# Optimization experiments

Hardware: AMD Instinct MI355X
Metric: run time of the kernel (lower is better)

The kernel has to match this reference:

```python
import jax, jax.numpy as jnp
import numpy as np

D = 1024          # feature dim (x_dim)
C = 32            # n classes (way)
SHOTS = 32
N_SUP = C * SHOTS
Q = 1024
REG = 0.5         # reg_param


def setup_inputs() -> dict:
    key = jax.random.key(0)
    ks = jax.random.split(key, 5)
    support_x = jax.random.normal(ks[0], (N_SUP, D), dtype=jnp.float32)
    query_x = jax.random.normal(ks[1], (Q, D), dtype=jnp.float32)
    labels_idx = (jnp.arange(N_SUP, dtype=jnp.int32) % C)  # every class present, equal shots
    m = jax.random.normal(ks[2], (1, D), dtype=jnp.float32) * 0.01
    kappa = jnp.float32(0.1)
    nu = jnp.float32(D)
    triu_diag = jnp.ones((D,), dtype=jnp.float32)
    triu_lower = jnp.eye(D, dtype=jnp.float32) + 0.01 * jax.random.normal(ks[3], (D, D), dtype=jnp.float32)
    return {"support_x": support_x, "query_x": query_x, "labels_idx": labels_idx,
            "m": m, "kappa": kappa, "nu": nu,
            "triu_diag": triu_diag, "triu_lower": triu_lower}


def _metaqda_fb(support_x, query_x, labels_idx, m, kappa, nu, triu_diag, triu_lower):
    onehot = jax.nn.one_hot(labels_idx, C, dtype=support_x.dtype)      # [N, C]
    Nj = jnp.sum(onehot, axis=0)                                       # [C]
    kappa_ = jnp.abs(kappa) + 1e-6
    nu_ = jnp.maximum(nu, jnp.float32(D - 1 + 1e-6))

    # Cholesky-factor prior scatter matrix: L @ L^T
    lower_mask = jnp.tril(jnp.ones((D, D), dtype=support_x.dtype), k=-1)
    L = jnp.diag(jnp.abs(triu_diag)) + triu_lower * lower_mask
    prior_S = L @ L.T                                                  # [D, D]

    # per-class sums (replaces python loop of rank-1 outer products with GEMMs)
    sum_x = onehot.T @ support_x                                       # [C, D]
    mean_x = sum_x / Nj[:, None]
    # sum_n x x^T per class: contract through [N,C,D] intermediate
    SXX = jnp.einsum('nc,nd,ne->cde', onehot, support_x, support_x)    # [C, D, D]

    kN = kappa_ + Nj                                                   # [C]
    mu = (kappa_ / kN)[:, None] * m + (Nj / kN)[:, None] * mean_x      # [C, D]

    mm = m.T @ m                                                       # [D, D]  (self_outer of [1,D])
    mumu = jnp.einsum('cd,ce->cde', mu, mu)                            # [C, D, D]
    S = prior_S[None] + SXX + kappa_ * mm[None] - kN[:, None, None] * mumu

    scale = (kN + 1.0) / ((nu_ + Nj - D + 1.0) * kN)                   # [C]
    sigma = S * scale[:, None, None]                                   # [C, D, D]

    sigma_inv = (1.0 - REG) * jnp.linalg.inv(sigma) + REG * jnp.eye(D, dtype=sigma.dtype)

    common = nu_ + Nj + 1.0 - D                                        # [C]
    _, logdet = jnp.linalg.slogdet(sigma)
    bias = (jax.lax.lgamma(0.5 * (common + D)) - jax.lax.lgamma(0.5 * common)
            - 0.5 * D * jnp.log(common) - 0.5 * logdet)                # [C]

    diff = query_x[:, None, :] - mu[None, :, :]                        # [Q, C, D]
    dist = jnp.einsum('qcd,cde,qce->qc', diff, sigma_inv, diff)        # [Q, C]
    preds = bias[None, :] - 0.5 * (common + D)[None, :] * jnp.log1p(dist / common[None, :])
    return preds


def reference(support_x, query_x, labels_idx, m, kappa, nu, triu_diag, triu_lower):
    return _metaqda_fb(support_x, query_x, labels_idx, m, kappa, nu, triu_diag, triu_lower)
```

## Files before the change

### kernel.cpp

```cpp
#include <hip/hip_runtime.h>
#include <math.h>

#define Dk 1024
#define Ck 32
#define Nk 1024
#define Qk 1024
#define REGP 0.5f
#define NB 64
#define NROWSV (Qk + Nk + Ck + 1)

#define CO_KAPPA 0
#define CO_NU    1
#define CO_NJ    2
#define CO_KN    34
#define CO_SCALE 66
#define CO_COMMON 98
#define CO_COEF  130
#define CO_BIASA 162
#define CO_BIASF 200

#define O_Y    0u
#define O_P    0u
#define O_W    2162688u
#define O_T    3211264u
#define O_MU   3473408u
#define O_QM   3506176u
#define O_MB   3538944u
#define O_MI   3578112u
#define O_QNY  3617280u
#define O_QNO  3618304u
#define O_MUN  3619328u
#define O_GMM  3619360u
#define O_EX   3619392u
#define O_CONS 3619408u
#define O_CIDX 3619664u
#define O_YH   3652432u
#define O_YM   4733776u
#define O_YL   5815120u
#define O_WH   6896464u
#define O_WM   7420752u
#define O_WL   7945040u
#define O_OH   8469328u
#define O_OM   9550672u
#define O_OL   10632016u

#define WS_DECL \
    float* Y     = Wbuf + O_Y;    (void)Y; \
    float* P     = Wbuf + O_P;    (void)P; \
    float* W     = Wbuf + O_W;    (void)W; \
    float* Tb    = Wbuf + O_T;    (void)Tb; \
    float* mu    = Wbuf + O_MU;   (void)mu; \
    float* QM    = Wbuf + O_QM;   (void)QM; \
    float* Mbuf  = Wbuf + O_MB;   (void)Mbuf; \
    float* Minv  = Wbuf + O_MI;   (void)Minv; \
    float* qny   = Wbuf + O_QNY;  (void)qny; \
    float* qno   = Wbuf + O_QNO;  (void)qno; \
    float* mun2o = Wbuf + O_MUN;  (void)mun2o; \
    float* gmm   = Wbuf + O_GMM;  (void)gmm; \
    float* extraf= Wbuf + O_EX;   (void)extraf; \
    float* cons  = Wbuf + O_CONS; (void)cons; \
    int*   cidx  = (int*)(Wbuf + O_CIDX); (void)cidx; \
    ushort* sYh = (ushort*)(Wbuf + O_YH); (void)sYh; \
    ushort* sYm = (ushort*)(Wbuf + O_YM); (void)sYm; \
    ushort* sYl = (ushort*)(Wbuf + O_YL); (void)sYl; \
    ushort* sWh = (ushort*)(Wbuf + O_WH); (void)sWh; \
    ushort* sWm = (ushort*)(Wbuf + O_WM); (void)sWm; \
    ushort* sWl = (ushort*)(Wbuf + O_WL); (void)sWl; \
    ushort* sOh = (ushort*)(Wbuf + O_OH); (void)sOh; \
    ushort* sOm = (ushort*)(Wbuf + O_OM); (void)sOm; \
    ushort* sOl = (ushort*)(Wbuf + O_OL); (void)sOl;

typedef __attribute__((ext_vector_type(8))) __bf16 bf16x8;
typedef __attribute__((ext_vector_type(4))) float f32x4;

#define MFMA(a, b, c) __builtin_amdgcn_mfma_f32_16x16x32_bf16(a, b, c, 0, 0, 0)

__device__ __forceinline__ ushort f2bf(float x) {
    unsigned u = __float_as_uint(x);
    return (ushort)((u + 0x7FFFu + ((u >> 16) & 1u)) >> 16);
}
__device__ __forceinline__ float bf2f(ushort h) {
    return __uint_as_float(((unsigned)h) << 16);
}

__device__ __forceinline__ float wave_red(float s) {
#pragma unroll
    for (int o = 32; o > 0; o >>= 1) s += __shfl_down(s, o, 64);
    return s;
}

#define LDSA(c, r, k8) ((c) * 5120 + (r) * 40 + (k8))
#define LDSB(c, r, k8) (15360 + (c) * 2560 + (r) * 40 + (k8))
#define LDS_HW 23040

__device__ __forceinline__ void tile_fetch(
    bf16x8* ra, bf16x8* rb,
    const ushort* Ah, const ushort* Am, const ushort* Al, int aRow0, int aRowMax,
    const ushort* Bh, const ushort* Bm, const ushort* Bl, int bRow0,
    int kcol, int t)
{
    bf16x8 z = {};
#pragma unroll
    for (int u = 0; u < 6; ++u) {
        const ushort* As = (u < 2) ? Ah : ((u < 4) ? Am : Al);
        int rem = ((u & 1) << 8) + t;
        int row = rem >> 2, kg = rem & 3;
        int gr = aRow0 + row;
        ra[u] = (gr < aRowMax) ? *(const bf16x8*)(As + (size_t)gr * 1024 + kcol + kg * 8) : z;
    }
#pragma unroll
    for (int u = 0; u < 3; ++u) {
        const ushort* Bs = (u == 0) ? Bh : ((u == 1) ? Bm : Bl);
        int row = t >> 2, kg = t & 3;
        rb[u] = *(const bf16x8*)(Bs + (size_t)(bRow0 + row) * 1024 + kcol + kg * 8);
    }
}

__device__ __forceinline__ void tile_store(ushort* lds, const bf16x8* ra, const bf16x8* rb, int t) {
#pragma unroll
    for (int u = 0; u < 6; ++u) {
        int rem = ((u & 1) << 8) + t;
        int row = rem >> 2, kg = rem & 3;
        *(bf16x8*)(lds + LDSA(u >> 1, row, kg * 8)) = ra[u];
    }
#pragma unroll
    for (int u = 0; u < 3; ++u) {
        int row = t >> 2, kg = t & 3;
        *(bf16x8*)(lds + LDSB(u, row, kg * 8)) = rb[u];
    }
}

__device__ __forceinline__ void tile_compute(const ushort* lds, f32x4 acc[2][4],
                                             int w, int lr, int lk) {
    bf16x8 af[2][3], bf_[4][3];
#pragma unroll
    for (int rf = 0; rf < 2; ++rf)
#pragma unroll
        for (int c = 0; c < 3; ++c)
            af[rf][c] = *(const bf16x8*)(lds + LDSA(c, w * 32 + rf * 16 + lr, lk * 8));
#pragma unroll
    for (int cf = 0; cf < 4; ++cf)
#pragma unroll
        for (int c = 0; c < 3; ++c)
            bf_[cf][c] = *(const bf16x8*)(lds + LDSB(c, cf * 16 + lr, lk * 8));
#pragma unroll
    for (int rf = 0; rf < 2; ++rf)
#pragma unroll
        for (int cf = 0; cf < 4; ++cf) {
            f32x4 a = acc[rf][cf];
            a = MFMA(af[rf][0], bf_[cf][0], a);
            a = MFMA(af[rf][0], bf_[cf][1], a);
            a = MFMA(af[rf][1], bf_[cf][0], a);
            a = MFMA(af[rf][0], bf_[cf][2], a);
            a = MFMA(af[rf][2], bf_[cf][0], a);
            a = MFMA(af[rf][1], bf_[cf][1], a);
            acc[rf][cf] = a;
        }
}

__device__ __forceinline__ void tile_gemm(
    ushort* lds, f32x4 acc[2][4],
    const ushort* Ah, const ushort* Am, const ushort* Al, int aRow0, int aRowMax,
    const ushort* Bh, const ushort* Bm, const ushort* Bl, int bRow0,
    int ksteps, int t)
{
    const int w = t >> 6, lr = t & 15, lk = (t >> 4) & 3;
    bf16x8 ra[6], rb[3];
    tile_fetch(ra, rb, Ah, Am, Al, aRow0, aRowMax, Bh, Bm, Bl, bRow0, 0, t);
    tile_store(lds, ra, rb, t);
    __syncthreads();
    for (int kt = 0; kt < ksteps; ++kt) {
        if (kt + 1 < ksteps)
            tile_fetch(ra, rb, Ah, Am, Al, aRow0, aRowMax, Bh, Bm, Bl, bRow0, (kt + 1) * 32, t);
        tile_compute(lds, acc, w, lr, lk);
        __syncthreads();
        if (kt + 1 < ksteps)
            tile_store(lds, ra, rb, t);
        __syncthreads();
    }
}

__device__ __forceinline__ void fetch4(float4* reg, const float* src, int ld,
                                       int rowbase, int rowmax, int colbase, int t) {
#pragma unroll
    for (int u = 0; u < 4; ++u) {
        int slot = t + u * 256;
        int r = slot >> 4, c4 = slot & 15;
        int gr = rowbase + r;
        reg[u] = (gr < rowmax) ? *(const float4*)(src + (size_t)gr * ld + colbase + c4 * 4)
                               : make_float4(0.f, 0.f, 0.f, 0.f);
    }
}
__device__ __forceinline__ void stT(float* dst, const float4* reg, int t) {
#pragma unroll
    for (int u = 0; u < 4; ++u) {
        int slot = t + u * 256;
        int r = slot >> 4, c4 = slot & 15;
        dst[(c4 * 4 + 0) * 68 + r] = reg[u].x;
        dst[(c4 * 4 + 1) * 68 + r] = reg[u].y;
        dst[(c4 * 4 + 2) * 68 + r] = reg[u].z;
        dst[(c4 * 4 + 3) * 68 + r] = reg[u].w;
    }
}
__device__ __forceinline__ void stN(float* dst, const float4* reg, int t) {
#pragma unroll
    for (int u = 0; u < 4; ++u) {
        int slot = t + u * 256;
        int r = slot >> 4, c4 = slot & 15;
        *(float4*)(dst + r * 68 + c4 * 4) = reg[u];
    }
}
__device__ __forceinline__ void gemm16(const float* At, const float* Bt,
                                       float acc[4][4], int tx, int ty) {
#pragma unroll 4
    for (int kk = 0; kk < NB; ++kk) {
        float4 a = *(const float4*)(At + kk * 68 + ty * 4);
        float4 b = *(const float4*)(Bt + kk * 68 + tx * 4);
        float av[4] = {a.x, a.y, a.z, a.w};
        float bv[4] = {b.x, b.y, b.z, b.w};
#pragma unroll
        for (int r = 0; r < 4; ++r)
#pragma unroll
            for (int s = 0; s < 4; ++s) acc[r][s] += av[r] * bv[s];
    }
}
__device__ __forceinline__ void mm_task(
    const float* aSrc, int aLd, int aRow, int aRowMax, int aCol, int aRowStep, int aColStep,
    const float* bSrc, int bLd, int bRow, int bRowMax, int bCol, int bRowStep, int bColStep,
    bool bTrans, int k0, int k1,
    float acc[4][4], float* smA, float* smB, int t, int tx, int ty)
{
    float4 ra[4], rb[4];
    fetch4(ra, aSrc, aLd, aRow + k0 * aRowStep, aRowMax, aCol + k0 * aColStep, t);
    fetch4(rb, bSrc, bLd, bRow + k0 * bRowStep, bRowMax, bCol + k0 * bColStep, t);
    stT(smA, ra, t);
    if (bTrans) stT(smB, rb, t); else stN(smB, rb, t);
    __syncthreads();
    for (int kt = k0; kt < k1; ++kt) {
        if (kt + 1 < k1) {
            fetch4(ra, aSrc, aLd, aRow + (kt + 1) * aRowStep, aRowMax, aCol + (kt + 1) * aColStep, t);
            fetch4(rb, bSrc, bLd, bRow + (kt + 1) * bRowStep, bRowMax, bCol + (kt + 1) * bColStep, t);
        }
        gemm16(smA, smB, acc, tx, ty);
        __syncthreads();
        if (kt + 1 < k1) {
            stT(smA, ra, t);
            if (bTrans) stT(smB, rb, t); else stN(smB, rb, t);
        }
        __syncthreads();
    }
}

__global__ __launch_bounds__(256) void k_p0(const float* qx, const int* labels,
                                            const float* mvec, const float* kappa,
                                            const float* nu, const float* td,
                                            const float* tl, float* Wbuf) {
    __shared__ __align__(16) float smem[9216];
    float* smA = smem;
    float* smB = smem + 4352;
    float* sX  = smem + 8704;
    WS_DECL
    const int t = threadIdx.x;
    const int lane = t & 63, wv = t >> 6;
    const int tau = blockIdx.x;

    if (tau == 0) {
        int* scnt = (int*)sX;
        if (t < Ck) scnt[t] = 0;
        __syncthreads();
        for (int n = t; n < Nk; n += 256) {
            int l = labels[n];
            int pos = atomicAdd(&scnt[l], 1);
            cidx[l * Nk + pos] = n;
        }
        __syncthreads();
        if (t < Ck) {
            float kap = fabsf(kappa[0]) + 1e-6f;
            float nu_ = fmaxf(nu[0], (float)(Dk - 1) + 1e-6f);
            float Njf = (float)scnt[t];
            float kN = kap + Njf;
            if (t == 0) { cons[CO_KAPPA] = kap; cons[CO_NU] = nu_; }
            cons[CO_NJ + t] = Njf;
            cons[CO_KN + t] = kN;
            cons[CO_SCALE + t] = (kN + 1.0f) / ((nu_ + Njf - (float)Dk + 1.0f) * kN);
            float common = nu_ + Njf + 1.0f - (float)Dk;
            cons[CO_COMMON + t] = common;
            cons[CO_COEF + t] = 0.5f * (common + (float)Dk);
            cons[CO_BIASA + t] = lgammaf(0.5f * (common + (float)Dk)) - lgammaf(0.5f * common)
                                 - 0.5f * (float)Dk * logf(common);
        }
    } else if (tau == 1) {
        float s = 0.f;
        for (int i = t; i < Dk; i += 256) s += logf(fabsf(td[i]));
        s = wave_red(s);
        if (lane == 0) sX[wv] = s;
        __syncthreads();
        if (t == 0) extraf[0] = 2.f * (sX[0] + sX[1] + sX[2] + sX[3]);
    } else if (tau < 18) {
        int I = tau - 2, b0 = I * NB;
        for (int idx = t; idx < NB * NB; idx += 256) {
            int r = idx >> 6, c = idx & 63;
            float v;
            if (c < r) v = tl[(size_t)(b0 + r) * Dk + b0 + c];
            else if (c == r) v = fabsf(td[b0 + r]);
            else v = 0.f;
            smA[r * 68 + c] = v;
        }
        __syncthreads();
        if (t < NB) {
            int j = t;
            smB[j * 68 + j] = 1.f / smA[j * 68 + j];
            for (int i = j + 1; i < NB; ++i) {
                float s = 0.f;
                for (int k = j; k < i; ++k) s += smA[i * 68 + k] * smB[k * 68 + j];
                smB[i * 68 + j] = -s / smA[i * 68 + i];
            }
        }
        __syncthreads();
        for (int idx = t; idx < NB * NB; idx += 256) {
            int r = idx >> 6, c = idx & 63;
            W[(size_t)(b0 + r) * Dk + b0 + c] = (c <= r) ? smB[r * 68 + c] : 0.f;
        }
    } else if (tau < 21) {
        int base = (tau - 18) * 13056;
        for (int i = t; i < 13056 && base + i < 39168; i += 256) Mbuf[base + i] = 0.f;
    } else if (tau == 21) {
        if (t < 32) { mun2o[t] = 0.f; gmm[t] = 0.f; }
    } else if (tau < 86) {
        int rbase = (tau - 22) * 16;
        for (int j = wv; j < 16; j += 4) {
            const float* row = qx + (size_t)(rbase + j) * Dk;
            float s = 0.f;
            for (int d = lane; d < Dk; d += 64) { float v = row[d]; s += v * v; }
            s = wave_red(s);
            if (lane == 0) qno[rbase + j] = s;
        }
    } else if (tau < 150) {
        int rbase = (tau - 86) * 16;
        for (int j = 0; j < 16; ++j) {
            int r = rbase + j;
            ((float4*)(Y + (size_t)r * Dk))[t] = ((const float4*)(qx + (size_t)r * Dk))[t];
        }
    } else if (tau == 150) {
        ((float4*)(Y + (size_t)(Qk + Nk + Ck) * Dk))[t] = ((const float4*)mvec)[t];
    } else {
        float4* z = (float4*)(Y + (size_t)2081 * Dk);
        for (int i = t; i < 31 * 256; i += 256) z[i] = make_float4(0, 0, 0, 0);
    }
}

__global__ __launch_bounds__(256) void k_p1(const float* sx, const float* mvec, float* Wbuf) {
    __shared__ float sX[512];
    WS_DECL
    const int t = threadIdx.x;
    const int lane = t & 63, wv = t >> 6;
    const int tau = blockIdx.x;
    if (tau < 128) {
        int c = tau >> 2;
        int d = ((tau & 3) << 8) + t;
        int Nj = (int)cons[CO_NJ + c];
        float kap = cons[CO_KAPPA], kN = cons[CO_KN + c];
        float acc = 0.f;
        for (int s = 0; s < Nj; ++s) acc += sx[(size_t)cidx[c * Nk + s] * Dk + d];
        float muv = (kap * mvec[d] + acc) / kN;
        mu[c * Dk + d] = muv;
        Y[(size_t)(Qk + Nk + c) * Dk + d] = muv;
        float s2 = wave_red(muv * muv);
        if (lane == 0) sX[wv] = s2;
        __syncthreads();
        if (t == 0) atomicAdd(&mun2o[c], sX[0] + sX[1] + sX[2] + sX[3]);
    } else {
        int rbase = (tau - 128) * 16;
        for (int j = 0; j < 16; ++j) {
            int n = rbase + j;
            int srcrow = cidx[(n >> 5) * Nk + (n & 31)];
            ((float4*)(Y + (size_t)(Qk + n) * Dk))[t] = ((const float4*)(sx + (size_t)srcrow * Dk))[t];
        }
    }
}

__global__ __launch_bounds__(256) void k_t1(const float* tl, float* Wbuf) {
    __shared__ __align__(16) float smem[8704];
    float* smA = smem;
    float* smB = smem + 4352;
    WS_DECL
    const int t = threadIdx.x;
    const int tx = t & 15, ty = t >> 4;
    const int BIG = 1 << 30;
    int pb = blockIdx.x * 128;
    float acc[4][4] = {};
    mm_task(tl, Dk, pb + 64, BIG, pb, 0, NB,
            W, Dk, pb, BIG, pb, NB, 0, false, 0, 1,
            acc, smA, smB, t, tx, ty);
    {
        float4 ra[4];
        fetch4(ra, W, Dk, pb + 64, BIG, pb + 64, t);
#pragma unroll
        for (int r = 0; r < 4; ++r)
#pragma unroll
            for (int s = 0; s < 4; ++s)
                smB[(ty * 4 + r) * 68 + tx * 4 + s] = acc[r][s];
        stT(smA, ra, t);
    }
    __syncthreads();
    float acc2[4][4] = {};
    gemm16(smA, smB, acc2, tx, ty);
    __syncthreads();
#pragma unroll
    for (int r = 0; r < 4; ++r)
#pragma unroll
        for (int s = 0; s < 4; ++s)
            W[(size_t)(pb + 64 + ty * 4 + r) * Dk + pb + tx * 4 + s] = -acc2[r][s];
}

__global__ __launch_bounds__(256) void k_tr_a(const float* tl, float* Wbuf, int h, int ht) {
    __shared__ __align__(16) float smem[8704];
    float* smA = smem;
    float* smB = smem + 4352;
    WS_DECL
    const int t = threadIdx.x;
    const int tx = t & 15, ty = t >> 4;
    const int BIG = 1 << 30;
    int tau = blockIdx.x;
    int p = tau / (ht * ht), rr = tau % (ht * ht);
    int i = rr / ht, j = rr % ht;
    int pb = p * 2 * h;
    float acc[4][4] = {};
    mm_task(tl, Dk, pb + h + i * NB, BIG, pb, 0, NB,
            W, Dk, pb, BIG, pb + j * NB, NB, 0, false, 0, ht,
            acc, smA, smB, t, tx, ty);
    float* Tp = Tb + (size_t)p * h * h;
#pragma unroll
    for (int r = 0; r < 4; ++r)
#pragma unroll
        for (int s = 0; s < 4; ++s)
            Tp[(size_t)(i * NB + ty * 4 + r) * h + j * NB + tx * 4 + s] = acc[r][s];
}

__global__ __launch_bounds__(256) void k_tr_b(float* Wbuf, int h, int ht) {
    __shared__ __align__(16) float smem[8704];
    float* smA = smem;
    float* smB = smem + 4352;
    WS_DECL
    const int t = threadIdx.x;
    const int tx = t & 15, ty = t >> 4;
    const int BIG = 1 << 30;
    int tau = blockIdx.x;
    int p = tau / (ht * ht), rr = tau % (ht * ht);
    int i = rr / ht, j = rr % ht;
    int pb = p * 2 * h;
    const float* Tp = Tb + (size_t)p * h * h;
    float acc[4][4] = {};
    mm_task(W, Dk, pb + h + i * NB, BIG, pb + h, 0, NB,
            Tp, h, 0, BIG, j * NB, NB, 0, false, 0, ht,
            acc, smA, smB, t, tx, ty);
#pragma unroll
    for (int r = 0; r < 4; ++r)
#pragma unroll
        for (int s = 0; s < 4; ++s)
            W[(size_t)(pb + h + i * NB + ty * 4 + r) * Dk + pb + j * NB + tx * 4 + s] = -acc[r][s];
}

__global__ __launch_bounds__(256) void k_cvt(float* Wbuf) {
    WS_DECL
    const int t = threadIdx.x;
#pragma unroll
    for (int u = 0; u < 4; ++u) {
        unsigned g = blockIdx.x * 1024u + u * 256u + t;
        bool isY = g < 540672u;
        float4 v = isY ? ((const float4*)Y)[g] : ((const float4*)W)[g - 540672u];
        ushort* ph = isY ? sYh : sWh;
        ushort* pm = isY ? sYm : sWm;
        ushort* pl = isY ? sYl : sWl;
        size_t o = (size_t)(isY ? g : (g - 540672u)) * 4;
        float vv[4] = {v.x, v.y, v.z, v.w};
        ushort4 H, M, L;
        ushort* Hp = (ushort*)&H; ushort* Mp = (ushort*)&M; ushort* Lp = (ushort*)&L;
#pragma unroll
        for (int c = 0; c < 4; ++c) {
            float x = vv[c];
            ushort h = f2bf(x);
            float r1 = x - bf2f(h);
            ushort m_ = f2bf(r1);
            ushort lo = f2bf(r1 - bf2f(m_));
            Hp[c] = h; Mp[c] = m_; Lp[c] = lo;
        }
        *(ushort4*)(ph + o) = H;
        *(ushort4*)(pm + o) = M;
        *(ushort4*)(pl + o) = L;
    }
}

__global__ __launch_bounds__(256) void k_yg(float* Wbuf) {
    __shared__ __align__(16) ushort lds[LDS_HW];
    WS_DECL
    const int t = threadIdx.x;
    int e = blockIdx.x;
    int jt = 15 - e / 17;
    int rt = e % 17;
    f32x4 acc[2][4] = {};
    tile_gemm(lds, acc, sYh, sYm, sYl, rt * 128, 2112,
              sWh, sWm, sWl, jt * 64, (jt + 1) * 2, t);
    const int w = t >> 6, lr = t & 15, lk = (t >> 4) & 3;
#pragma unroll
    for (int rf = 0; rf < 2; ++rf)
#pragma unroll
        for (int cf = 0; cf < 4; ++cf)
#pragma unroll
            for (int r = 0; r < 4; ++r) {
                int grow = rt * 128 + w * 32 + rf * 16 + lk * 4 + r;
                if (grow < NROWSV) {
                    float v = acc[rf][cf][r];
                    size_t o = (size_t)grow * 1024 + jt * 64 + cf * 16 + lr;
                    ushort h = f2bf(v);
                    float r1 = v - bf2f(h);
                    ushort m_ = f2bf(r1);
                    ushort lo = f2bf(r1 - bf2f(m_));
                    sOh[o] = h; sOm[o] = m_; sOl[o] = lo;
                }
            }
}

__global__ __launch_bounds__(256) void k_p4m(float* Wbuf) {
    __shared__ __align__(16) ushort lds[LDS_HW];
    WS_DECL
    const int t = threadIdx.x;
    int e = blockIdx.x;
    f32x4 acc[2][4] = {};
    const int w = t >> 6, lr = t & 15, lk = (t >> 4) & 3;
    if (e < 144) {
        int mt = e / 16, qt = e % 16;
        tile_gemm(lds, acc, sOh, sOm, sOl, 1024 + mt * 128, 2081,
                  sOh, sOm, sOl, qt * 64, 32, t);
#pragma unroll
        for (int rf = 0; rf < 2; ++rf)
#pragma unroll
            for (int cf = 0; cf < 4; ++cf)
#pragma unroll
                for (int r = 0; r < 4; ++r) {
                    int n = mt * 128 + w * 32 + rf * 16 + lk * 4 + r;
                    if (n < Nk + Ck + 1)
                        P[(size_t)n * 1024 + qt * 64 + cf * 16 + lr] = acc[rf][cf][r];
                }
    } else {
        int qt = e - 144;
        tile_gemm(lds, acc, sYh, sYm, sYl, 2048, 2080,
                  sYh, sYm, sYl, qt * 64, 32, t);
#pragma unroll
        for (int rf = 0; rf < 2; ++rf)
#pragma unroll
            for (int cf = 0; cf < 4; ++cf)
#pragma unroll
                for (int r = 0; r < 4; ++r) {
                    int rq = w * 32 + rf * 16 + lk * 4 + r;
                    if (rq < 32)
                        QM[(size_t)rq * 1024 + qt * 64 + cf * 16 + lr] = acc[rf][cf][r];
                }
    }
}

__global__ __launch_bounds__(256) void k_gram(float* Wbuf) {
    __shared__ __align__(16) float smA[34 * 68];
    WS_DECL
    const int t = threadIdx.x;
    const int lane = t & 63, wv = t >> 6;
    const int tau = blockIdx.x;
    if (tau < 128) {
        int c = tau >> 2, kc = tau & 3;
        float accg[5];
        int iu[5], ju[5];
#pragma unroll
        for (int u = 0; u < 5; ++u) {
            int e = t + u * 256;
            iu[u] = e / 34; ju[u] = e - iu[u] * 34;
            accg[u] = 0.f;
        }
        for (int kt = kc * 4; kt < kc * 4 + 4; ++kt) {
            for (int e2 = t; e2 < 34 * NB; e2 += 256) {
                int i = e2 >> 6, k = e2 & 63;
                int yr = (i < 32) ? (Qk + c * 32 + i) : ((i == 32) ? (Qk + Nk + c) : (Qk + Nk + Ck));
                size_t o = (size_t)yr * 1024 + kt * NB + k;
                smA[i * 68 + k] = bf2f(sOh[o]) + bf2f(sOm[o]) + bf2f(sOl[o]);
            }
            __syncthreads();
#pragma unroll
            for (int u = 0; u < 5; ++u) {
                int e = t + u * 256;
                if (e < 1156) {
                    float s = 0.f;
                    for (int k = 0; k < NB; ++k) s += smA[iu[u] * 68 + k] * smA[ju[u] * 68 + k];
                    accg[u] += s;
                }
            }
            __syncthreads();
        }
#pragma unroll
        for (int u = 0; u < 5; ++u) {
            int e = t + u * 256;
            if (e < 1156)
                atomicAdd(&Mbuf[c * 1224 + iu[u] * 36 + ju[u]], accg[u]);
        }
    } else {
        int rbase = (tau - 128) * 16;
        for (int j = wv; j < 16; j += 4) {
            size_t ro = (size_t)(rbase + j) * 1024;
            float s = 0.f;
            for (int d = lane; d < Dk; d += 64) {
                size_t o = ro + d;
                float v = bf2f(sOh[o]) + bf2f(sOm[o]) + bf2f(sOl[o]);
                s += v * v;
            }
            s = wave_red(s);
            if (lane == 0) qny[rbase + j] = s;
        }
    }
}

__global__ __launch_bounds__(256) void k_p5(float* Wbuf) {
    __shared__ float smem[2464];
    float* Ml = smem;
    float* Z  = smem + 1200;
    float* Dv = smem + 2400;
    WS_DECL
    const int t = threadIdx.x;
    const int c = blockIdx.x;
    float kN = cons[CO_KN + c], kap = cons[CO_KAPPA];
    for (int e = t; e < 34 * 34; e += 256) {
        int i = e / 34, j = e - i * 34;
        Ml[i * 35 + j] = Mbuf[c * 1224 + i * 36 + j];
    }
    __syncthreads();
    if (t == 0) {
        gmm[c] = Ml[32 * 35 + 32];
        Ml[32 * 35 + 32] += -1.f / kN;
        Ml[33 * 35 + 33] += 1.f / kap;
    }
    if (t < 32) Ml[t * 35 + t] += 1.f;
    __syncthreads();
    for (int j = 0; j < 34; ++j) {
        if (t == 0) {
            float s = Ml[j * 35 + j];
            for (int k = 0; k < j; ++k) s -= Ml[j * 35 + k] * Ml[j * 35 + k] * Dv[k];
            Dv[j] = s;
        }
        __syncthreads();
        if (t > j && t < 34) {
            float s = Ml[t * 35 + j];
            for (int k = 0; k < j; ++k) s -= Ml[t * 35 + k] * Ml[j * 35 + k] * Dv[k];
            Ml[t * 35 + j] = s / Dv[j];
        }
        __syncthreads();
    }
    if (t < 34) {
        for (int i = 0; i < 34; ++i) {
            float s = (i == t) ? 1.f : 0.f;
            for (int k = 0; k < i; ++k) s -= Ml[i * 35 + k] * Z[k * 35 + t];
            Z[i * 35 + t] = s;
        }
        for (int i = 33; i >= 0; --i) {
            float s = Z[i * 35 + t] / Dv[i];
            for (int k = i + 1; k < 34; ++k) s -= Ml[k * 35 + i] * Z[k * 35 + t];
            Z[i * 35 + t] = s;
        }
    }
    __syncthreads();
    for (int e = t; e < 34 * 34; e += 256) {
        int i = e / 34, j = e - i * 34;
        Minv[c * 1224 + i * 36 + j] = Z[i * 35 + j];
    }
    if (t == 0) {
        float ld = 0.f;
        for (int j = 0; j < 34; ++j) ld += logf(fabsf(Dv[j]));
        float scale = cons[CO_SCALE + c];
        float logdet = (float)Dk * logf(scale) + extraf[0] + logf(kN) + logf(kap) + ld;
        cons[CO_BIASF + c] = cons[CO_BIASA + c] - 0.5f * logdet;
    }
}

__global__ __launch_bounds__(256) void k_p6(float* Wbuf, float* out) {
    __shared__ __align__(16) float smem[3904];
    float* Mi  = smem;
    float* wL  = smem + 1200;
    float* gsm = smem + 3520;
    float* red = smem + 3520 + 128;
    WS_DECL
    const int t = threadIdx.x;
    const int tau = blockIdx.x;
    int qt = tau >> 5, c = tau & 31;
    for (int e = t; e < 34 * 34; e += 256) {
        int i = e / 34, j = e - i * 34;
        Mi[i * 35 + j] = Minv[c * 1224 + i * 36 + j];
    }
    if (t < 34)
        gsm[t] = (t < 32) ? Mbuf[c * 1224 + t * 36 + 32]
                          : ((t == 32) ? gmm[c] : Mbuf[c * 1224 + 33 * 36 + 32]);
    __syncthreads();
    for (int e = t; e < 34 * NB; e += 256) {
        int i = e >> 6, qq = e & 63;
        int prow = (i < 32) ? (c * 32 + i) : ((i == 32) ? (Nk + c) : (Nk + Ck));
        wL[i * 68 + qq] = P[(size_t)prow * Qk + qt * NB + qq] - gsm[i];
    }
    __syncthreads();
    {
        int q = t & 63, part = t >> 6;
        int start = (part < 2) ? part * 9 : 18 + (part - 2) * 8;
        int cnt = (part < 2) ? 9 : 8;
        float partial = 0.f;
        for (int i = start; i < start + cnt; ++i) {
            float v = 0.f;
            for (int j = 0; j < 34; ++j) v += Mi[i * 35 + j] * wL[j * 68 + q];
            partial += v * wL[i * 68 + q];
        }
        red[part * 64 + q] = partial;
    }
    __syncthreads();
    if (t < 64) {
        int q = t;
        float quad = red[q] + red[64 + q] + red[128 + q] + red[192 + q];
        int qg = qt * NB + q;
        float w32 = wL[32 * 68 + q];
        float ydist2 = qny[qg] - 2.f * w32 - gmm[c];
        float dd = qno[qg] + mun2o[c] - 2.f * QM[(size_t)c * Qk + qg];
        float scale = cons[CO_SCALE + c], common = cons[CO_COMMON + c];
        float dist = (1.f - REGP) / scale * (ydist2 - quad) + REGP * dd;
        out[(size_t)qg * Ck + c] = cons[CO_BIASF + c] - cons[CO_COEF + c] * log1pf(dist / common);
    }
}

extern "C" void kernel_launch(void* const* d_in, const int* in_sizes, int n_in,
                              void* d_out, int out_size, void* d_ws, size_t ws_size,
                              hipStream_t stream) {
    const float* sx = (const float*)d_in[0];
    const float* qx = (const float*)d_in[1];
    const int* labels = (const int*)d_in[2];
    const float* mvec = (const float*)d_in[3];
    const float* kappa = (const float*)d_in[4];
    const float* nu = (const float*)d_in[5];
    const float* td = (const float*)d_in[6];
    const float* tl = (const float*)d_in[7];
    float* W = (float*)d_ws;
    float* out = (float*)d_out;

    hipLaunchKernelGGL(k_p0, dim3(152), dim3(256), 0, stream,
                       qx, labels, mvec, kappa, nu, td, tl, W);
    hipLaunchKernelGGL(k_p1, dim3(192), dim3(256), 0, stream, sx, mvec, W);
    hipLaunchKernelGGL(k_t1, dim3(8), dim3(256), 0, stream, tl, W);
    for (int l = 2; l <= 4; ++l) {
        int h = 32 << l, ht = h >> 6, pairs = 16 >> l;
        int nt = pairs * ht * ht;
        hipLaunchKernelGGL(k_tr_a, dim3(nt), dim3(256), 0, stream, tl, W, h, ht);
        hipLaunchKernelGGL(k_tr_b, dim3(nt), dim3(256), 0, stream, W, h, ht);
    }
    hipLaunchKernelGGL(k_cvt, dim3(784), dim3(256), 0, stream, W);
    hipLaunchKernelGGL(k_yg, dim3(272), dim3(256), 0, stream, W);
    hipLaunchKernelGGL(k_p4m, dim3(160), dim3(256), 0, stream, W);
    hipLaunchKernelGGL(k_gram, dim3(192), dim3(256), 0, stream, W);
    hipLaunchKernelGGL(k_p5, dim3(32), dim3(256), 0, stream, W);
    hipLaunchKernelGGL(k_p6, dim3(512), dim3(256), 0, stream, W, out);
}
```

Before: 407.1 us.

## Fuse bf16 splitting into producers, use 8-wave GEMM tiles and split-K with atomics

Several ideas are combined. Query, support, mu and m rows are split into three bf16 parts directly in the producer kernels instead of being staged in fp32 and converted by a separate pass, so the conversion kernel now only handles W. The 64-row diagonal-block triangular inverse is rewritten as a register-resident per-column forward substitution. The MFMA GEMMs move to 512-thread blocks with one 16-row fragment per wave, with a block-index swizzle. The P GEMM is split four ways along K and accumulates into a P buffer zeroed by k_p0 using atomicAdd. The aim is fewer memory passes and more blocks in flight, at the cost of atomic traffic and non-deterministic summation order.

```diff
diff --git a/kernel.cpp b/kernel.cpp
--- a/kernel.cpp
+++ b/kernel.cpp
@@ -19,7 +19,6 @@
 #define CO_BIASA 162
 #define CO_BIASF 200
 
-#define O_Y    0u
 #define O_P    0u
 #define O_W    2162688u
 #define O_T    3211264u
@@ -45,11 +44,9 @@
 #define O_OL   10632016u
 
 #define WS_DECL \
-    float* Y     = Wbuf + O_Y;    (void)Y; \
     float* P     = Wbuf + O_P;    (void)P; \
     float* W     = Wbuf + O_W;    (void)W; \
     float* Tb    = Wbuf + O_T;    (void)Tb; \
-    float* mu    = Wbuf + O_MU;   (void)mu; \
     float* QM    = Wbuf + O_QM;   (void)QM; \
     float* Mbuf  = Wbuf + O_MB;   (void)Mbuf; \
     float* Minv  = Wbuf + O_MI;   (void)Minv; \
@@ -82,6 +79,23 @@
 __device__ __forceinline__ float bf2f(ushort h) {
     return __uint_as_float(((unsigned)h) << 16);
 }
+__device__ __forceinline__ void split1(float x, ushort& h, ushort& m, ushort& l) {
+    h = f2bf(x);
+    float r1 = x - bf2f(h);
+    m = f2bf(r1);
+    l = f2bf(r1 - bf2f(m));
+}
+__device__ __forceinline__ void split_store4(ushort* ph, ushort* pm, ushort* pl,
+                                             size_t o, float4 v) {
+    float vv[4] = {v.x, v.y, v.z, v.w};
+    ushort4 H, M, L;
+    ushort* Hp = (ushort*)&H; ushort* Mp = (ushort*)&M; ushort* Lp = (ushort*)&L;
+#pragma unroll
+    for (int c = 0; c < 4; ++c) split1(vv[c], Hp[c], Mp[c], Lp[c]);
+    *(ushort4*)(ph + o) = H;
+    *(ushort4*)(pm + o) = M;
+    *(ushort4*)(pl + o) = L;
+}
 
 __device__ __forceinline__ float wave_red(float s) {
 #pragma unroll
@@ -93,89 +107,91 @@
 #define LDSB(c, r, k8) (15360 + (c) * 2560 + (r) * 40 + (k8))
 #define LDS_HW 23040
 
-__device__ __forceinline__ void tile_fetch(
+__device__ __forceinline__ void tile_fetch8(
     bf16x8* ra, bf16x8* rb,
     const ushort* Ah, const ushort* Am, const ushort* Al, int aRow0, int aRowMax,
     const ushort* Bh, const ushort* Bm, const ushort* Bl, int bRow0,
     int kcol, int t)
 {
     bf16x8 z = {};
-#pragma unroll
-    for (int u = 0; u < 6; ++u) {
-        const ushort* As = (u < 2) ? Ah : ((u < 4) ? Am : Al);
-        int rem = ((u & 1) << 8) + t;
-        int row = rem >> 2, kg = rem & 3;
+    int row = t >> 2, kg = t & 3;
+#pragma unroll
+    for (int u = 0; u < 3; ++u) {
+        const ushort* As = (u == 0) ? Ah : ((u == 1) ? Am : Al);
         int gr = aRow0 + row;
         ra[u] = (gr < aRowMax) ? *(const bf16x8*)(As + (size_t)gr * 1024 + kcol + kg * 8) : z;
     }
 #pragma unroll
-    for (int u = 0; u < 3; ++u) {
-        const ushort* Bs = (u == 0) ? Bh : ((u == 1) ? Bm : Bl);
-        int row = t >> 2, kg = t & 3;
-        rb[u] = *(const bf16x8*)(Bs + (size_t)(bRow0 + row) * 1024 + kcol + kg * 8);
-    }
-}
-
-__device__ __forceinline__ void tile_store(ushort* lds, const bf16x8* ra, const bf16x8* rb, int t) {
-#pragma unroll
-    for (int u = 0; u < 6; ++u) {
-        int rem = ((u & 1) << 8) + t;
-        int row = rem >> 2, kg = rem & 3;
-        *(bf16x8*)(lds + LDSA(u >> 1, row, kg * 8)) = ra[u];
-    }
-#pragma unroll
-    for (int u = 0; u < 3; ++u) {
-        int row = t >> 2, kg = t & 3;
-        *(bf16x8*)(lds + LDSB(u, row, kg * 8)) = rb[u];
-    }
-}
-
-__device__ __forceinline__ void tile_compute(const ushort* lds, f32x4 acc[2][4],
-                                             int w, int lr, int lk) {
-    bf16x8 af[2][3], bf_[4][3];
-#pragma unroll
-    for (int rf = 0; rf < 2; ++rf)
-#pragma unroll
-        for (int c = 0; c < 3; ++c)
-            af[rf][c] = *(const bf16x8*)(lds + LDSA(c, w * 32 + rf * 16 + lr, lk * 8));
+    for (int u = 0; u < 2; ++u) {
+        int slot = t + u * 512;
+        if (slot < 768) {
+            int comp = slot >> 8, rem = slot & 255;
+            int br = rem >> 2, bkg = rem & 3;
+            const ushort* Bs = (comp == 0) ? Bh : ((comp == 1) ? Bm : Bl);
+            rb[u] = *(const bf16x8*)(Bs + (size_t)(bRow0 + br) * 1024 + kcol + bkg * 8);
+        }
+    }
+}
+
+__device__ __forceinline__ void tile_store8(ushort* lds, const bf16x8* ra, const bf16x8* rb, int t) {
+    int row = t >> 2, kg = t & 3;
+#pragma unroll
+    for (int u = 0; u < 3; ++u)
+        *(bf16x8*)(lds + LDSA(u, row, kg * 8)) = ra[u];
+#pragma unroll
+    for (int u = 0; u < 2; ++u) {
+        int slot = t + u * 512;
+        if (slot < 768) {
+            int comp = slot >> 8, rem = slot & 255;
+            int br = rem >> 2, bkg = rem & 3;
+            *(bf16x8*)(lds + LDSB(comp, br, bkg * 8)) = rb[u];
+        }
+    }
+}
+
+__device__ __forceinline__ void tile_compute8(const ushort* lds, f32x4 acc[4],
+                                              int w, int lr, int lk) {
+    bf16x8 af[3], bf_[4][3];
+#pragma unroll
+    for (int c = 0; c < 3; ++c)
+        af[c] = *(const bf16x8*)(lds + LDSA(c, w * 16 + lr, lk * 8));
 #pragma unroll
     for (int cf = 0; cf < 4; ++cf)
 #pragma unroll
         for (int c = 0; c < 3; ++c)
             bf_[cf][c] = *(const bf16x8*)(lds + LDSB(c, cf * 16 + lr, lk * 8));
 #pragma unroll
-    for (int rf = 0; rf < 2; ++rf)
-#pragma unroll
-        for (int cf = 0; cf < 4; ++cf) {
-            f32x4 a = acc[rf][cf];
-            a = MFMA(af[rf][0], bf_[cf][0], a);
-            a = MFMA(af[rf][0], bf_[cf][1], a);
-            a = MFMA(af[rf][1], bf_[cf][0], a);
-            a = MFMA(af[rf][0], bf_[cf][2], a);
-            a = MFMA(af[rf][2], bf_[cf][0], a);
-            a = MFMA(af[rf][1], bf_[cf][1], a);
-            acc[rf][cf] = a;
-        }
-}
-
-__device__ __forceinline__ void tile_gemm(
-    ushort* lds, f32x4 acc[2][4],
+    for (int cf = 0; cf < 4; ++cf) {
+        f32x4 a = acc[cf];
+        a = MFMA(af[0], bf_[cf][0], a);
+        a = MFMA(af[0], bf_[cf][1], a);
+        a = MFMA(af[1], bf_[cf][0], a);
+        a = MFMA(af[0], bf_[cf][2], a);
+        a = MFMA(af[2], bf_[cf][0], a);
+        a = MFMA(af[1], bf_[cf][1], a);
+        acc[cf] = a;
+    }
+}
+
+__device__ __forceinline__ void tile_gemm8(
+    ushort* lds, f32x4 acc[4],
     const ushort* Ah, const ushort* Am, const ushort* Al, int aRow0, int aRowMax,
     const ushort* Bh, const ushort* Bm, const ushort* Bl, int bRow0,
-    int ksteps, int t)
+    int kbase, int ksteps, int t)
 {
     const int w = t >> 6, lr = t & 15, lk = (t >> 4) & 3;
-    bf16x8 ra[6], rb[3];
-    tile_fetch(ra, rb, Ah, Am, Al, aRow0, aRowMax, Bh, Bm, Bl, bRow0, 0, t);
-    tile_store(lds, ra, rb, t);
+    bf16x8 ra[3], rb[2];
+    tile_fetch8(ra, rb, Ah, Am, Al, aRow0, aRowMax, Bh, Bm, Bl, bRow0, kbase * 32, t);
+    tile_store8(lds, ra, rb, t);
     __syncthreads();
     for (int kt = 0; kt < ksteps; ++kt) {
         if (kt + 1 < ksteps)
-            tile_fetch(ra, rb, Ah, Am, Al, aRow0, aRowMax, Bh, Bm, Bl, bRow0, (kt + 1) * 32, t);
-        tile_compute(lds, acc, w, lr, lk);
+            tile_fetch8(ra, rb, Ah, Am, Al, aRow0, aRowMax, Bh, Bm, Bl, bRow0,
+                        (kbase + kt + 1) * 32, t);
+        tile_compute8(lds, acc, w, lr, lk);
         __syncthreads();
         if (kt + 1 < ksteps)
-            tile_store(lds, ra, rb, t);
+            tile_store8(lds, ra, rb, t);
         __syncthreads();
     }
 }
@@ -257,7 +273,6 @@
                                             const float* tl, float* Wbuf) {
     __shared__ __align__(16) float smem[9216];
     float* smA = smem;
-    float* smB = smem + 4352;
     float* sX  = smem + 8704;
     WS_DECL
     const int t = threadIdx.x;
@@ -297,29 +312,34 @@
         __syncthreads();
         if (t == 0) extraf[0] = 2.f * (sX[0] + sX[1] + sX[2] + sX[3]);
     } else if (tau < 18) {
-        int I = tau - 2, b0 = I * NB;
-        for (int idx = t; idx < NB * NB; idx += 256) {
-            int r = idx >> 6, c = idx & 63;
-            float v;
-            if (c < r) v = tl[(size_t)(b0 + r) * Dk + b0 + c];
-            else if (c == r) v = fabsf(td[b0 + r]);
-            else v = 0.f;
-            smA[r * 68 + c] = v;
-        }
-        __syncthreads();
-        if (t < NB) {
-            int j = t;
-            smB[j * 68 + j] = 1.f / smA[j * 68 + j];
-            for (int i = j + 1; i < NB; ++i) {
-                float s = 0.f;
-                for (int k = j; k < i; ++k) s += smA[i * 68 + k] * smB[k * 68 + j];
-                smB[i * 68 + j] = -s / smA[i * 68 + i];
+        int b0 = (tau - 2) * NB;
+        for (int idx = t; idx < 64 * 64; idx += 256) {
+            int m = idx >> 6, i = idx & 63;
+            smem[i * 72 + m] = (m > i) ? tl[(size_t)(b0 + m) * Dk + b0 + i] : 0.f;
+        }
+        if (t < 64) smem[4608 + t] = 1.f / fabsf(td[b0 + t]);
+        __syncthreads();
+        if (t < 64) {
+            const int j = t;
+            float r[64];
+#pragma unroll
+            for (int m = 0; m < 64; ++m) r[m] = (m == j) ? 1.f : 0.f;
+#pragma unroll
+            for (int i = 0; i < 64; ++i) {
+                float x = r[i] * smem[4608 + i];
+                r[i] = x;
+#pragma unroll
+                for (int g = (i >> 2); g < 16; ++g) {
+                    float4 lt = *(const float4*)&smem[i * 72 + g * 4];
+                    r[g * 4 + 0] -= lt.x * x;
+                    r[g * 4 + 1] -= lt.y * x;
+                    r[g * 4 + 2] -= lt.z * x;
+                    r[g * 4 + 3] -= lt.w * x;
+                }
             }
-        }
-        __syncthreads();
-        for (int idx = t; idx < NB * NB; idx += 256) {
-            int r = idx >> 6, c = idx & 63;
-            W[(size_t)(b0 + r) * Dk + b0 + c] = (c <= r) ? smB[r * 68 + c] : 0.f;
+#pragma unroll
+            for (int i = 0; i < 64; ++i)
+                W[(size_t)(b0 + i) * Dk + b0 + j] = r[i];
         }
     } else if (tau < 21) {
         int base = (tau - 18) * 13056;
@@ -339,13 +359,16 @@
         int rbase = (tau - 86) * 16;
         for (int j = 0; j < 16; ++j) {
             int r = rbase + j;
-            ((float4*)(Y + (size_t)r * Dk))[t] = ((const float4*)(qx + (size_t)r * Dk))[t];
+            float4 v = ((const float4*)(qx + (size_t)r * Dk))[t];
+            split_store4(sYh, sYm, sYl, (size_t)r * 1024 + (size_t)t * 4, v);
         }
     } else if (tau == 150) {
-        ((float4*)(Y + (size_t)(Qk + Nk + Ck) * Dk))[t] = ((const float4*)mvec)[t];
+        float4 v = ((const float4*)mvec)[t];
+        split_store4(sYh, sYm, sYl, (size_t)2080 * 1024 + (size_t)t * 4, v);
     } else {
-        float4* z = (float4*)(Y + (size_t)2081 * Dk);
-        for (int i = t; i < 31 * 256; i += 256) z[i] = make_float4(0, 0, 0, 0);
+        int rbase = (tau - 151) * 16;
+        for (int j = 0; j < 16; ++j)
+            ((float4*)(P + (size_t)(rbase + j) * 1024))[t] = make_float4(0, 0, 0, 0);
     }
 }
 
@@ -363,8 +386,10 @@
         float acc = 0.f;
         for (int s = 0; s < Nj; ++s) acc += sx[(size_t)cidx[c * Nk + s] * Dk + d];
         float muv = (kap * mvec[d] + acc) / kN;
-        mu[c * Dk + d] = muv;
-        Y[(size_t)(Qk + Nk + c) * Dk + d] = muv;
+        size_t o = (size_t)(2048 + c) * 1024 + d;
+        ushort h, m_, l_;
+        split1(muv, h, m_, l_);
+        sYh[o] = h; sYm[o] = m_; sYl[o] = l_;
         float s2 = wave_red(muv * muv);
         if (lane == 0) sX[wv] = s2;
         __syncthreads();
@@ -374,7 +399,8 @@
         for (int j = 0; j < 16; ++j) {
             int n = rbase + j;
             int srcrow = cidx[(n >> 5) * Nk + (n & 31)];
-            ((float4*)(Y + (size_t)(Qk + n) * Dk))[t] = ((const float4*)(sx + (size_t)srcrow * Dk))[t];
+            float4 v = ((const float4*)(sx + (size_t)srcrow * Dk))[t];
+            split_store4(sYh, sYm, sYl, (size_t)(1024 + n) * 1024 + (size_t)t * 4, v);
         }
     }
 }
@@ -461,101 +487,75 @@
             W[(size_t)(pb + h + i * NB + ty * 4 + r) * Dk + pb + j * NB + tx * 4 + s] = -acc[r][s];
 }
 
-__global__ __launch_bounds__(256) void k_cvt(float* Wbuf) {
+__global__ __launch_bounds__(256) void k_cvtw(float* Wbuf) {
     WS_DECL
     const int t = threadIdx.x;
 #pragma unroll
     for (int u = 0; u < 4; ++u) {
         unsigned g = blockIdx.x * 1024u + u * 256u + t;
-        bool isY = g < 540672u;
-        float4 v = isY ? ((const float4*)Y)[g] : ((const float4*)W)[g - 540672u];
-        ushort* ph = isY ? sYh : sWh;
-        ushort* pm = isY ? sYm : sWm;
-        ushort* pl = isY ? sYl : sWl;
-        size_t o = (size_t)(isY ? g : (g - 540672u)) * 4;
-        float vv[4] = {v.x, v.y, v.z, v.w};
-        ushort4 H, M, L;
-        ushort* Hp = (ushort*)&H; ushort* Mp = (ushort*)&M; ushort* Lp = (ushort*)&L;
-#pragma unroll
-        for (int c = 0; c < 4; ++c) {
-            float x = vv[c];
-            ushort h = f2bf(x);
-            float r1 = x - bf2f(h);
-            ushort m_ = f2bf(r1);
-            ushort lo = f2bf(r1 - bf2f(m_));
-            Hp[c] = h; Mp[c] = m_; Lp[c] = lo;
-        }
-        *(ushort4*)(ph + o) = H;
-        *(ushort4*)(pm + o) = M;
-        *(ushort4*)(pl + o) = L;
-    }
-}
-
-__global__ __launch_bounds__(256) void k_yg(float* Wbuf) {
+        float4 v = ((const float4*)W)[g];
+        split_store4(sWh, sWm, sWl, (size_t)g * 4, v);
+    }
+}
+
+__global__ __launch_bounds__(512) void k_yg(float* Wbuf) {
     __shared__ __align__(16) ushort lds[LDS_HW];
     WS_DECL
     const int t = threadIdx.x;
-    int e = blockIdx.x;
-    int jt = 15 - e / 17;
-    int rt = e % 17;
-    f32x4 acc[2][4] = {};
-    tile_gemm(lds, acc, sYh, sYm, sYl, rt * 128, 2112,
-              sWh, sWm, sWl, jt * 64, (jt + 1) * 2, t);
+    int b = blockIdx.x;
+    int s = (b & 7) * 34 + (b >> 3);
+    int jt = 15 - s / 17, rt = s % 17;
+    f32x4 acc[4] = {};
+    tile_gemm8(lds, acc, sYh, sYm, sYl, rt * 128, 2081,
+               sWh, sWm, sWl, jt * 64, 0, (jt + 1) * 2, t);
     const int w = t >> 6, lr = t & 15, lk = (t >> 4) & 3;
 #pragma unroll
-    for (int rf = 0; rf < 2; ++rf)
+    for (int cf = 0; cf < 4; ++cf)
+#pragma unroll
+        for (int r = 0; r < 4; ++r) {
+            int grow = rt * 128 + w * 16 + lk * 4 + r;
+            if (grow < NROWSV) {
+                size_t o = (size_t)grow * 1024 + jt * 64 + cf * 16 + lr;
+                ushort h, m_, l_;
+                split1(acc[cf][r], h, m_, l_);
+                sOh[o] = h; sOm[o] = m_; sOl[o] = l_;
+            }
+        }
+}
+
+__global__ __launch_bounds__(512) void k_p4m(float* Wbuf) {
+    __shared__ __align__(16) ushort lds[LDS_HW];
+    WS_DECL
+    const int t = threadIdx.x;
+    int b = blockIdx.x;
+    int s = (b & 7) * 74 + (b >> 3);
+    const int w = t >> 6, lr = t & 15, lk = (t >> 4) & 3;
+    f32x4 acc[4] = {};
+    if (s < 576) {
+        int qt = s / 36, rem = s % 36;
+        int mt = rem >> 2, kc = rem & 3;
+        tile_gemm8(lds, acc, sOh, sOm, sOl, 1024 + mt * 128, 2081,
+                   sOh, sOm, sOl, qt * 64, kc * 8, 8, t);
 #pragma unroll
         for (int cf = 0; cf < 4; ++cf)
 #pragma unroll
             for (int r = 0; r < 4; ++r) {
-                int grow = rt * 128 + w * 32 + rf * 16 + lk * 4 + r;
-                if (grow < NROWSV) {
-                    float v = acc[rf][cf][r];
-                    size_t o = (size_t)grow * 1024 + jt * 64 + cf * 16 + lr;
-                    ushort h = f2bf(v);
-                    float r1 = v - bf2f(h);
-                    ushort m_ = f2bf(r1);
-                    ushort lo = f2bf(r1 - bf2f(m_));
-                    sOh[o] = h; sOm[o] = m_; sOl[o] = lo;
-                }
+                int n = mt * 128 + w * 16 + lk * 4 + r;
+                if (n < Nk + Ck + 1)
+                    atomicAdd(&P[(size_t)n * 1024 + qt * 64 + cf * 16 + lr], acc[cf][r]);
             }
-}
-
-__global__ __launch_bounds__(256) void k_p4m(float* Wbuf) {
-    __shared__ __align__(16) ushort lds[LDS_HW];
-    WS_DECL
-    const int t = threadIdx.x;
-    int e = blockIdx.x;
-    f32x4 acc[2][4] = {};
-    const int w = t >> 6, lr = t & 15, lk = (t >> 4) & 3;
-    if (e < 144) {
-        int mt = e / 16, qt = e % 16;
-        tile_gemm(lds, acc, sOh, sOm, sOl, 1024 + mt * 128, 2081,
-                  sOh, sOm, sOl, qt * 64, 32, t);
-#pragma unroll
-        for (int rf = 0; rf < 2; ++rf)
-#pragma unroll
-            for (int cf = 0; cf < 4; ++cf)
-#pragma unroll
-                for (int r = 0; r < 4; ++r) {
-                    int n = mt * 128 + w * 32 + rf * 16 + lk * 4 + r;
-                    if (n < Nk + Ck + 1)
-                        P[(size_t)n * 1024 + qt * 64 + cf * 16 + lr] = acc[rf][cf][r];
-                }
     } else {
-        int qt = e - 144;
-        tile_gemm(lds, acc, sYh, sYm, sYl, 2048, 2080,
-                  sYh, sYm, sYl, qt * 64, 32, t);
-#pragma unroll
-        for (int rf = 0; rf < 2; ++rf)
-#pragma unroll
-            for (int cf = 0; cf < 4; ++cf)
-#pragma unroll
-                for (int r = 0; r < 4; ++r) {
-                    int rq = w * 32 + rf * 16 + lk * 4 + r;
-                    if (rq < 32)
-                        QM[(size_t)rq * 1024 + qt * 64 + cf * 16 + lr] = acc[rf][cf][r];
-                }
+        int qt = s - 576;
+        tile_gemm8(lds, acc, sYh, sYm, sYl, 2048, 2081,
+                   sYh, sYm, sYl, qt * 64, 0, 32, t);
+#pragma unroll
+        for (int cf = 0; cf < 4; ++cf)
+#pragma unroll
+            for (int r = 0; r < 4; ++r) {
+                int rq = w * 16 + lk * 4 + r;
+                if (rq < 32)
+                    QM[(size_t)rq * 1024 + qt * 64 + cf * 16 + lr] = acc[cf][r];
+            }
     }
 }
 
@@ -741,7 +741,7 @@
     float* W = (float*)d_ws;
     float* out = (float*)d_out;
 
-    hipLaunchKernelGGL(k_p0, dim3(152), dim3(256), 0, stream,
+    hipLaunchKernelGGL(k_p0, dim3(219), dim3(256), 0, stream,
                        qx, labels, mvec, kappa, nu, td, tl, W);
     hipLaunchKernelGGL(k_p1, dim3(192), dim3(256), 0, stream, sx, mvec, W);
     hipLaunchKernelGGL(k_t1, dim3(8), dim3(256), 0, stream, tl, W);
@@ -751,9 +751,9 @@
         hipLaunchKernelGGL(k_tr_a, dim3(nt), dim3(256), 0, stream, tl, W, h, ht);
         hipLaunchKernelGGL(k_tr_b, dim3(nt), dim3(256), 0, stream, W, h, ht);
     }
-    hipLaunchKernelGGL(k_cvt, dim3(784), dim3(256), 0, stream, W);
-    hipLaunchKernelGGL(k_yg, dim3(272), dim3(256), 0, stream, W);
-    hipLaunchKernelGGL(k_p4m, dim3(160), dim3(256), 0, stream, W);
+    hipLaunchKernelGGL(k_cvtw, dim3(256), dim3(256), 0, stream, W);
+    hipLaunchKernelGGL(k_yg, dim3(272), dim3(512), 0, stream, W);
+    hipLaunchKernelGGL(k_p4m, dim3(592), dim3(512), 0, stream, W);
     hipLaunchKernelGGL(k_gram, dim3(192), dim3(256), 0, stream, W);
     hipLaunchKernelGGL(k_p5, dim3(32), dim3(256), 0, stream, W);
     hipLaunchKernelGGL(k_p6, dim3(512), dim3(256), 0, stream, W, out);
```

Result: no change. 412.1 us (+1.2%).
